# Kernel optimization log

Hardware: AMD Instinct MI355X
Metric: run time of the kernel (lower is better)

Reference implementation:

```python
import jax, jax.numpy as jnp
import numpy as np

B, S, D, H = 4, 2048, 1024, 16
HEAD_DIM = D // H
THETA = 10000.0
NEG_INF = -1e10


def apply_rope(x, theta=THETA):
    # RoPE over the FULL hid_dim (applied before head split, as in the torch code)
    d = x.shape[-1]
    s = x.shape[1]
    freqs = 1.0 / theta ** (jnp.arange(0, d, 2, dtype=jnp.float32) / d)  # [d/2]
    ang = jnp.arange(s, dtype=jnp.float32)[:, None] * freqs[None, :]     # [s, d/2]
    cos, sin = jnp.cos(ang), jnp.sin(ang)
    xr = x.reshape(x.shape[0], s, d // 2, 2)
    re, im = xr[..., 0], xr[..., 1]
    # complex multiply (re + i*im) * (cos + i*sin)
    out = jnp.stack([re * cos - im * sin, re * sin + im * cos], axis=-1)
    return out.reshape(x.shape)


def setup_inputs() -> dict:
    key = jax.random.key(0)
    ks = jax.random.split(key, 8)
    w_scale = 0.02
    return {
        "query": jax.random.normal(ks[0], (B, S, D), jnp.float32),
        "key": jax.random.normal(ks[1], (B, S, D), jnp.float32),
        "value": jax.random.normal(ks[2], (B, S, D), jnp.float32),
        "Wq": jax.random.normal(ks[3], (D, D), jnp.float32) * w_scale,
        "bq": jnp.zeros((D,), jnp.float32),
        "Wk": jax.random.normal(ks[4], (D, D), jnp.float32) * w_scale,
        "bk": jnp.zeros((D,), jnp.float32),
        "Wv": jax.random.normal(ks[5], (D, D), jnp.float32) * w_scale,
        "bv": jnp.zeros((D,), jnp.float32),
        "Wo": jax.random.normal(ks[6], (D, D), jnp.float32) * w_scale,
        "bo": jnp.zeros((D,), jnp.float32),
        "mask": jax.random.randint(ks[7], (B, 1, 1, S), 0, 2, jnp.int32),
    }


def reference(query, key, value, Wq, bq, Wk, bk, Wv, bv, Wo, bo, mask):
    b = query.shape[0]
    Q = query @ Wq + bq  # [B,Sq,D]
    K = key @ Wk + bk    # [B,Sk,D]
    V = value @ Wv + bv  # [B,Sk,D]
    Q = apply_rope(Q)
    K = apply_rope(K)
    # split heads: [B,H,S,head_dim]
    Qh = Q.reshape(b, -1, H, HEAD_DIM).transpose(0, 2, 1, 3)
    Kh = K.reshape(b, -1, H, HEAD_DIM).transpose(0, 2, 1, 3)
    Vh = V.reshape(b, -1, H, HEAD_DIM).transpose(0, 2, 1, 3)
    scale = 1.0 / jnp.sqrt(jnp.float32(HEAD_DIM))
    energy = jnp.einsum("bhqd,bhkd->bhqk", Qh, Kh) * scale
    energy = jnp.where(mask == 0, NEG_INF, energy)
    attn = jax.nn.softmax(energy, axis=-1)
    x = jnp.einsum("bhqk,bhkd->bhqd", attn, Vh)
    x = x.transpose(0, 2, 1, 3).reshape(b, -1, D)
    return x @ Wo + bo
```

## Files before the change

### kernel.cpp

```cpp
#include <hip/hip_runtime.h>
#include <math.h>

#define S_LEN 2048
#define DMODEL 1024
#define NHEAD 16
#define HDIM 64

typedef unsigned short ushort_t;
typedef __attribute__((ext_vector_type(8))) short short8;
typedef __attribute__((ext_vector_type(4))) float floatx4;
typedef __attribute__((ext_vector_type(4))) unsigned short ushort4v;
typedef __attribute__((ext_vector_type(2))) unsigned short ushort2v;

typedef __attribute__((address_space(3))) unsigned int lds_uint;
typedef const __attribute__((address_space(1))) unsigned int gbl_uint;

__device__ __forceinline__ float b2f(ushort_t u) {
  return __uint_as_float(((unsigned)u) << 16);
}
__device__ __forceinline__ ushort_t f2b(float x) {
  unsigned u = __float_as_uint(x);
  return (ushort_t)((u + 0x7fffu + ((u >> 16) & 1u)) >> 16);
}
__device__ __forceinline__ void gld16(const void* g, void* l) {
  __builtin_amdgcn_global_load_lds((gbl_uint*)g, (lds_uint*)l, 16, 0, 0);
}

__global__ __launch_bounds__(256) void detect_kernel(
    const unsigned* __restrict__ q, int* __restrict__ flag) {
  __shared__ int cnt[256];
  int c = 0;
#pragma unroll
  for (int i = 0; i < 16; ++i) {
    const unsigned w = q[threadIdx.x * 16 + i];
    const unsigned e = (w >> 7) & 0xFFu;
    c += (e >= 112u && e <= 135u) ? 1 : 0;
  }
  cnt[threadIdx.x] = c;
  __syncthreads();
  if (threadIdx.x == 0) {
    int t = 0;
    for (int i = 0; i < 256; ++i) t += cnt[i];
    *flag = (t > 2048) ? 1 : 0;
  }
}

__global__ __launch_bounds__(256) void bias_kernel(
    const void* __restrict__ bq, const void* __restrict__ bk,
    const void* __restrict__ bv, const void* __restrict__ bo,
    const int* __restrict__ flag, float* __restrict__ out) {
  const int i = blockIdx.x * 256 + threadIdx.x;
  const int z = i >> 10;
  const void* src = z == 0 ? bq : z == 1 ? bk : z == 2 ? bv : bo;
  const int j = i & 1023;
  const float v = (*flag) ? b2f(((const ushort_t*)src)[j])
                          : ((const float*)src)[j];
  out[i] = v;
}

__global__ __launch_bounds__(256) void wtrans_kernel(
    const void* __restrict__ Wq, const void* __restrict__ Wk,
    const void* __restrict__ Wv, const void* __restrict__ Wo,
    const int* __restrict__ flag, ushort_t* __restrict__ Wt) {
  __shared__ float t[32][33];
  const void* src = blockIdx.z == 0 ? Wq : blockIdx.z == 1 ? Wk
                    : blockIdx.z == 2 ? Wv : Wo;
  ushort_t* dst = Wt + (size_t)blockIdx.z * (DMODEL * (size_t)DMODEL);
  const int isbf = *flag;
  const int tx = threadIdx.x & 31, ty = threadIdx.x >> 5;
  const int bx = blockIdx.x * 32, by = blockIdx.y * 32;
#pragma unroll
  for (int i = 0; i < 4; ++i) {
    const size_t idx = (size_t)(by + ty + 8 * i) * DMODEL + bx + tx;
    t[ty + 8 * i][tx] = isbf ? b2f(((const ushort_t*)src)[idx])
                             : ((const float*)src)[idx];
  }
  __syncthreads();
#pragma unroll
  for (int i = 0; i < 4; ++i)
    dst[(size_t)(bx + ty + 8 * i) * DMODEL + by + tx] = f2b(t[tx][ty + 8 * i]);
}

__global__ __launch_bounds__(256) void qkv_kernel(
    const void* __restrict__ qin, const void* __restrict__ kin,
    const void* __restrict__ vin, const ushort_t* __restrict__ Wt,
    const float* __restrict__ Bias, const int* __restrict__ flag,
    ushort_t* __restrict__ Qh, ushort_t* __restrict__ Kh,
    ushort_t* __restrict__ Vh) {
  const int z = blockIdx.z;
  const void* A = z == 0 ? qin : z == 1 ? kin : vin;
  const ushort_t* W = Wt + (size_t)z * (DMODEL * (size_t)DMODEL);
  ushort_t* dst = z == 0 ? Qh : z == 1 ? Kh : Vh;
  const int isbf = *flag;

  __shared__ __align__(16) ushort_t smem[2 * 128 * 64];
  ushort_t* As = smem;
  ushort_t* Bs = smem + 128 * 64;

  const int tid = threadIdx.x;
  const int w = tid >> 6, l = tid & 63;
  const int m0 = blockIdx.x * 128, n0 = blockIdx.y * 128;

  floatx4 acc[4][4] = {};

  const int lr8 = l >> 3, lc8 = l & 7;
  const int gblk = lc8 ^ lr8;
  const ushort_t* Agb =
      (const ushort_t*)A + (size_t)(m0 + w * 32 + lr8) * DMODEL + gblk * 8;
  const float* Agf =
      (const float*)A + (size_t)(m0 + w * 32 + (l >> 4)) * DMODEL + (l & 15) * 4;
  const ushort_t* Bg = W + (size_t)(n0 + w * 32 + lr8) * DMODEL + gblk * 8;
  ushort_t* Asw = As + (w * 32) * 64;
  ushort_t* Bsw = Bs + (w * 32) * 64;

  const int wm = (w >> 1) * 64, wn = (w & 1) * 64;
  const int lm = l & 15, lg = l >> 4;
  const int swz = lm & 7;
  const int cA0 = ((0 + lg) ^ swz) * 8;
  const int cA1 = ((4 + lg) ^ swz) * 8;

  for (int kt = 0; kt < 16; ++kt) {
    const int ko = kt * 64;
    if (isbf) {
#pragma unroll
      for (int i = 0; i < 4; ++i)
        gld16(Agb + (size_t)(i * 8) * DMODEL + ko, Asw + (i * 8) * 64);
    } else {
#pragma unroll
      for (int i = 0; i < 8; ++i) {
        const floatx4 x = *(const floatx4*)(Agf + (size_t)(i * 4) * DMODEL + ko);
        ushort4v h;
        h[0] = f2b(x.x); h[1] = f2b(x.y); h[2] = f2b(x.z); h[3] = f2b(x.w);
        const int row = i * 4 + (l >> 4);
        const int blk = ((l & 15) >> 1) ^ (row & 7);
        *(ushort4v*)&Asw[row * 64 + blk * 8 + (l & 1) * 4] = h;
      }
    }
#pragma unroll
    for (int i = 0; i < 4; ++i)
      gld16(Bg + (size_t)(i * 8) * DMODEL + ko, Bsw + (i * 8) * 64);
    __syncthreads();
#pragma unroll
    for (int kk = 0; kk < 64; kk += 32) {
      const int ck = kk ? cA1 : cA0;
      short8 af[4], bf[4];
#pragma unroll
      for (int t = 0; t < 4; ++t)
        af[t] = *(const short8*)&As[(wm + t * 16 + lm) * 64 + ck];
#pragma unroll
      for (int t = 0; t < 4; ++t)
        bf[t] = *(const short8*)&Bs[(wn + t * 16 + lm) * 64 + ck];
#pragma unroll
      for (int mt = 0; mt < 4; ++mt)
#pragma unroll
        for (int nt = 0; nt < 4; ++nt)
          acc[mt][nt] = __builtin_amdgcn_mfma_f32_16x16x32_bf16(
              af[mt], bf[nt], acc[mt][nt], 0, 0, 0);
    }
    __syncthreads();
  }

  ushort_t* ep = smem + w * 4096;
#pragma unroll
  for (int nt = 0; nt < 4; ++nt) {
    const int c = nt * 16 + lm;
    const float bval = Bias[z * DMODEL + n0 + wn + c];
#pragma unroll
    for (int mt = 0; mt < 4; ++mt)
#pragma unroll
      for (int r = 0; r < 4; ++r) {
        const int row_t = mt * 16 + lg * 4 + r;
        ep[row_t * 64 + ((((c >> 3) ^ (row_t & 7)) << 3) | (c & 7))] =
            f2b(acc[mt][nt][r] + bval);
      }
  }
  const int mg = m0 + wm;
  const int b_ = mg >> 11, s_base = mg & (S_LEN - 1);
  const int h_ = (n0 + wn) >> 6;
  ushort_t* dstb = dst + (((size_t)(b_ * NHEAD + h_) * S_LEN + s_base) << 6);
#pragma unroll
  for (int i = 0; i < 8; ++i) {
    const int row = lr8 + 8 * i;
    const short8 v = *(const short8*)&ep[row * 64 + ((lc8 ^ lr8) << 3)];
    *(short8*)(dstb + (size_t)row * 64 + lc8 * 8) = v;
  }
}

__global__ __launch_bounds__(256) void rope_kernel(ushort_t* __restrict__ QK) {
  const size_t p = (size_t)blockIdx.x * 256 + threadIdx.x;
  const int d2 = (int)(p & 31) * 2;
  const int s = (int)(p >> 5) & (S_LEN - 1);
  const int h = (int)(p >> 16) & (NHEAD - 1);
  const int n = h * HDIM + d2;
  const float freq = exp2f((float)n * (-13.287712379549449f / 1024.0f));
  float sn, cs;
  __sincosf((float)s * freq, &sn, &cs);
  ushort2v v = *(ushort2v*)(QK + 2 * p);
  const float re = b2f(v[0]), im = b2f(v[1]);
  ushort2v o;
  o[0] = f2b(re * cs - im * sn);
  o[1] = f2b(re * sn + im * cs);
  *(ushort2v*)(QK + 2 * p) = o;
}

__global__ __launch_bounds__(256) void vtrans_kernel(
    const ushort_t* __restrict__ V, ushort_t* __restrict__ Vt) {
  __shared__ ushort_t t[32][34];
  const int bh = blockIdx.z;
  const int s0 = blockIdx.x * 32, d0 = blockIdx.y * 32;
  const ushort_t* src = V + (size_t)bh * S_LEN * HDIM;
  ushort_t* dst = Vt + (size_t)bh * S_LEN * HDIM;
  const int tx = threadIdx.x & 31, ty = threadIdx.x >> 5;
#pragma unroll
  for (int i = 0; i < 4; ++i)
    t[ty + 8 * i][tx] = src[(size_t)(s0 + ty + 8 * i) * HDIM + d0 + tx];
  __syncthreads();
#pragma unroll
  for (int i = 0; i < 4; ++i)
    dst[(size_t)(d0 + ty + 8 * i) * S_LEN + s0 + tx] = t[tx][ty + 8 * i];
}

__global__ __launch_bounds__(256) void attn_kernel(
    const ushort_t* __restrict__ Qh, const ushort_t* __restrict__ Kh,
    const ushort_t* __restrict__ Vt, const int* __restrict__ mask,
    ushort_t* __restrict__ Xa) {
  const int nlin = blockIdx.y * 16 + blockIdx.x;
  const int bh = ((nlin & 7) << 3) | ((nlin >> 3) & 7);
  const int q0 = (nlin >> 6) * 128;
  const int b = bh >> 4, h = bh & 15;
  const int tid = threadIdx.x;
  const int w = tid >> 6, lane = tid & 63;
  const int lm = lane & 15, lg = lane >> 4;

  __shared__ __align__(16) ushort_t Ks[64 * 64];
  __shared__ __align__(16) ushort_t Vs[64 * 64];
  __shared__ __align__(16) ushort_t Ps[4][32 * 72];

  const ushort_t* Qb = Qh + ((size_t)bh * S_LEN + q0 + w * 32) * HDIM;
  const ushort_t* Kb = Kh + (size_t)bh * S_LEN * HDIM;
  const ushort_t* Vb = Vt + (size_t)bh * S_LEN * HDIM;
  const int* mb = mask + b * S_LEN;

  short8 qf[2][2];
#pragma unroll
  for (int mb_ = 0; mb_ < 2; ++mb_)
#pragma unroll
    for (int ks = 0; ks < 2; ++ks)
      qf[mb_][ks] = *(const short8*)(Qb + (size_t)(mb_ * 16 + lm) * HDIM +
                                     ks * 32 + lg * 8);

  const int lr8 = lane >> 3, lc8 = lane & 7;
  const int gblk = lc8 ^ lr8;
  const ushort_t* Kg = Kb + (size_t)(w * 16 + lr8) * HDIM + gblk * 8;
  const ushort_t* Vg = Vb + (size_t)(w * 16 + lr8) * S_LEN + gblk * 8;
  ushort_t* KsW = Ks + (w * 16) * 64;
  ushort_t* VsW = Vs + (w * 16) * 64;

  const int swz = lm & 7;
  const int cK0 = ((0 + lg) ^ swz) * 8;
  const int cK1 = ((4 + lg) ^ swz) * 8;

  floatx4 Oacc[2][5] = {};

  const short8 ones = {0x3F80, 0x3F80, 0x3F80, 0x3F80,
                       0x3F80, 0x3F80, 0x3F80, 0x3F80};

  for (int j0 = 0; j0 < S_LEN; j0 += 64) {
    __syncthreads();
    gld16(Kg + (size_t)j0 * HDIM, KsW);
    gld16(Kg + (size_t)(j0 + 8) * HDIM, KsW + 8 * 64);
    gld16(Vg + j0, VsW);
    gld16(Vg + (size_t)8 * S_LEN + j0, VsW + 8 * 64);
    int mj[4];
#pragma unroll
    for (int nb = 0; nb < 4; ++nb) mj[nb] = mb[j0 + nb * 16 + lm];
    __syncthreads();

    floatx4 Sacc[2][4] = {};
#pragma unroll
    for (int ks = 0; ks < 2; ++ks) {
      const int ck = ks ? cK1 : cK0;
      short8 kf[4];
#pragma unroll
      for (int nb = 0; nb < 4; ++nb)
        kf[nb] = *(const short8*)&Ks[(nb * 16 + lm) * 64 + ck];
#pragma unroll
      for (int mb_ = 0; mb_ < 2; ++mb_)
#pragma unroll
        for (int nb = 0; nb < 4; ++nb)
          Sacc[mb_][nb] = __builtin_amdgcn_mfma_f32_16x16x32_bf16(
              qf[mb_][ks], kf[nb], Sacc[mb_][nb], 0, 0, 0);
    }

#pragma unroll
    for (int mb_ = 0; mb_ < 2; ++mb_)
#pragma unroll
      for (int nb = 0; nb < 4; ++nb)
#pragma unroll
        for (int r = 0; r < 4; ++r) {
          const float sv = Sacc[mb_][nb][r] * 0.125f;
          const float p = __expf(mj[nb] ? sv : -50.0f);
          Ps[w][(mb_ * 16 + lg * 4 + r) * 72 + nb * 16 + lm] = f2b(p);
        }

#pragma unroll
    for (int ks = 0; ks < 2; ++ks) {
      const int ck = ks ? cK1 : cK0;
      short8 pf[2], vf[4];
#pragma unroll
      for (int mb_ = 0; mb_ < 2; ++mb_)
        pf[mb_] =
            *(const short8*)&Ps[w][(mb_ * 16 + lm) * 72 + ks * 32 + lg * 8];
#pragma unroll
      for (int nb = 0; nb < 4; ++nb)
        vf[nb] = *(const short8*)&Vs[(nb * 16 + lm) * 64 + ck];
#pragma unroll
      for (int mb_ = 0; mb_ < 2; ++mb_) {
#pragma unroll
        for (int nb = 0; nb < 4; ++nb)
          Oacc[mb_][nb] = __builtin_amdgcn_mfma_f32_16x16x32_bf16(
              pf[mb_], vf[nb], Oacc[mb_][nb], 0, 0, 0);
        Oacc[mb_][4] = __builtin_amdgcn_mfma_f32_16x16x32_bf16(
            pf[mb_], ones, Oacc[mb_][4], 0, 0, 0);
      }
    }
  }

#pragma unroll
  for (int mb_ = 0; mb_ < 2; ++mb_)
#pragma unroll
    for (int r = 0; r < 4; ++r) {
      const float inv = 1.0f / Oacc[mb_][4][r];
      const int q = q0 + w * 32 + mb_ * 16 + lg * 4 + r;
      ushort_t* orow = Xa + (size_t)(b * S_LEN + q) * DMODEL + h * HDIM;
#pragma unroll
      for (int nb = 0; nb < 4; ++nb)
        orow[nb * 16 + lm] = f2b(Oacc[mb_][nb][r] * inv);
    }
}

__global__ __launch_bounds__(256) void oproj_kernel(
    const ushort_t* __restrict__ X, const ushort_t* __restrict__ Wt,
    const float* __restrict__ BiasO, const int* __restrict__ flag,
    void* __restrict__ out) {
  const int isbf = *flag;
  __shared__ __align__(16) ushort_t smem[2 * 128 * 64];
  ushort_t* As = smem;
  ushort_t* Bs = smem + 128 * 64;
  const int tid = threadIdx.x;
  const int w = tid >> 6, l = tid & 63;
  const int m0 = blockIdx.x * 128, n0 = blockIdx.y * 128;

  floatx4 acc[4][4] = {};

  const int lr8 = l >> 3, lc8 = l & 7;
  const int gblk = lc8 ^ lr8;
  const ushort_t* Ag =
      X + (size_t)(m0 + w * 32 + lr8) * DMODEL + gblk * 8;
  const ushort_t* Bg =
      Wt + (size_t)(n0 + w * 32 + lr8) * DMODEL + gblk * 8;
  ushort_t* Asw = As + (w * 32) * 64;
  ushort_t* Bsw = Bs + (w * 32) * 64;

  const int wm = (w >> 1) * 64, wn = (w & 1) * 64;
  const int lm = l & 15, lg = l >> 4;
  const int swz = lm & 7;
  const int cA0 = ((0 + lg) ^ swz) * 8;
  const int cA1 = ((4 + lg) ^ swz) * 8;

  for (int kt = 0; kt < 16; ++kt) {
    const int ko = kt * 64;
#pragma unroll
    for (int i = 0; i < 4; ++i) {
      gld16(Ag + (size_t)(i * 8) * DMODEL + ko, Asw + (i * 8) * 64);
      gld16(Bg + (size_t)(i * 8) * DMODEL + ko, Bsw + (i * 8) * 64);
    }
    __syncthreads();
#pragma unroll
    for (int kk = 0; kk < 64; kk += 32) {
      const int ck = kk ? cA1 : cA0;
      short8 af[4], bf[4];
#pragma unroll
      for (int t = 0; t < 4; ++t)
        af[t] = *(const short8*)&As[(wm + t * 16 + lm) * 64 + ck];
#pragma unroll
      for (int t = 0; t < 4; ++t)
        bf[t] = *(const short8*)&Bs[(wn + t * 16 + lm) * 64 + ck];
#pragma unroll
      for (int mt = 0; mt < 4; ++mt)
#pragma unroll
        for (int nt = 0; nt < 4; ++nt)
          acc[mt][nt] = __builtin_amdgcn_mfma_f32_16x16x32_bf16(
              af[mt], bf[nt], acc[mt][nt], 0, 0, 0);
    }
    __syncthreads();
  }

  if (isbf) {
    ushort_t* ep = smem + w * 4096;
#pragma unroll
    for (int nt = 0; nt < 4; ++nt) {
      const int c = nt * 16 + lm;
      const float bval = BiasO[n0 + wn + c];
#pragma unroll
      for (int mt = 0; mt < 4; ++mt)
#pragma unroll
        for (int r = 0; r < 4; ++r) {
          const int row_t = mt * 16 + lg * 4 + r;
          ep[row_t * 64 + ((((c >> 3) ^ (row_t & 7)) << 3) | (c & 7))] =
              f2b(acc[mt][nt][r] + bval);
        }
    }
    ushort_t* outb = (ushort_t*)out + (size_t)(m0 + wm) * DMODEL + n0 + wn;
#pragma unroll
    for (int i = 0; i < 8; ++i) {
      const int row = lr8 + 8 * i;
      const short8 v = *(const short8*)&ep[row * 64 + ((lc8 ^ lr8) << 3)];
      *(short8*)(outb + (size_t)row * DMODEL + lc8 * 8) = v;
    }
  } else {
    const int lr = lg * 4;
#pragma unroll
    for (int nt = 0; nt < 4; ++nt) {
      const int n_g = n0 + wn + nt * 16 + lm;
      const float bval = BiasO[n_g];
#pragma unroll
      for (int mt = 0; mt < 4; ++mt)
#pragma unroll
        for (int r = 0; r < 4; ++r) {
          const int m_g = m0 + wm + mt * 16 + lr + r;
          ((float*)out)[(size_t)m_g * DMODEL + n_g] = acc[mt][nt][r] + bval;
        }
    }
  }
}

extern "C" void kernel_launch(void* const* d_in, const int* in_sizes, int n_in,
                              void* d_out, int out_size, void* d_ws,
                              size_t ws_size, hipStream_t stream) {
  char* ws = (char*)d_ws;
  const size_t MB = 1024 * 1024;
  int* flag = (int*)ws;
  float* Bias = (float*)(ws + 4096);
  ushort_t* Wt = (ushort_t*)(ws + 1 * MB);
  ushort_t* Qh = (ushort_t*)(ws + 16 * MB);
  ushort_t* Kh = (ushort_t*)(ws + 32 * MB);
  ushort_t* Vh = (ushort_t*)(ws + 48 * MB);
  ushort_t* Vt = (ushort_t*)(ws + 64 * MB);
  ushort_t* Xa = Vh;

  detect_kernel<<<1, 256, 0, stream>>>((const unsigned*)d_in[0], flag);
  bias_kernel<<<16, 256, 0, stream>>>(d_in[4], d_in[6], d_in[8], d_in[10],
                                      flag, Bias);
  wtrans_kernel<<<dim3(32, 32, 4), 256, 0, stream>>>(d_in[3], d_in[5], d_in[7],
                                                     d_in[9], flag, Wt);
  qkv_kernel<<<dim3(64, 8, 3), 256, 0, stream>>>(d_in[0], d_in[1], d_in[2], Wt,
                                                 Bias, flag, Qh, Kh, Vh);
  rope_kernel<<<32768, 256, 0, stream>>>(Qh);
  vtrans_kernel<<<dim3(64, 2, 64), 256, 0, stream>>>(Vh, Vt);
  attn_kernel<<<dim3(16, 64), 256, 0, stream>>>(Qh, Kh, Vt,
                                                (const int*)d_in[11], Xa);
  oproj_kernel<<<dim3(64, 8), 256, 0, stream>>>(
      Xa, Wt + (size_t)3 * DMODEL * DMODEL, Bias + 3 * DMODEL, flag, d_out);
}
```

Before: 440.6 us.

## Add pre-converted bf16 inputs and 256x256 pipelined QKV GEMM kernel

Adds a convert pass that writes q/k/v as bf16 into workspace, then replaces the 128-tile QKV projection with a 256x256-tile, 512-thread GEMM. The new GEMM double-buffers global-to-LDS loads with explicit waitcnt/barrier scheduling, uses a swizzled LDS layout and block-index swizzling, and writes head-split output through an LDS-staged epilogue. The aim is more data reuse per tile and better MFMA utilisation. In exchange it spends an extra pass and bandwidth on conversion, and the path runs only when the workspace is at least 128MB.

```diff
diff --git a/kernel.cpp b/kernel.cpp
--- a/kernel.cpp
+++ b/kernel.cpp
@@ -79,6 +79,207 @@
 #pragma unroll
   for (int i = 0; i < 4; ++i)
     dst[(size_t)(bx + ty + 8 * i) * DMODEL + by + tx] = f2b(t[tx][ty + 8 * i]);
+}
+
+__global__ __launch_bounds__(256) void convert_kernel(
+    const void* __restrict__ q, const void* __restrict__ k,
+    const void* __restrict__ v, const int* __restrict__ flag,
+    ushort_t* __restrict__ Abf) {
+  const int z = blockIdx.y;
+  const void* src = z == 0 ? q : z == 1 ? k : v;
+  ushort_t* dst = Abf + (size_t)z * (8192 * (size_t)DMODEL);
+  const size_t i = (size_t)blockIdx.x * 256 + threadIdx.x;
+  short8 o;
+  if (*flag) {
+    o = ((const short8*)src)[i];
+  } else {
+    const floatx4 a = ((const floatx4*)src)[2 * i];
+    const floatx4 b = ((const floatx4*)src)[2 * i + 1];
+    o[0] = (short)f2b(a.x); o[1] = (short)f2b(a.y);
+    o[2] = (short)f2b(a.z); o[3] = (short)f2b(a.w);
+    o[4] = (short)f2b(b.x); o[5] = (short)f2b(b.y);
+    o[6] = (short)f2b(b.z); o[7] = (short)f2b(b.w);
+  }
+  ((short8*)dst)[i] = o;
+}
+
+__device__ __forceinline__ void gemm256_core(
+    const ushort_t* __restrict__ A, const ushort_t* __restrict__ Bm,
+    const int m0, const int n0, ushort_t* smem, floatx4 acc[8][4]) {
+  const int tid = threadIdx.x;
+  const int w = tid >> 6, l = tid & 63;
+  const int wr = w >> 2, wc = w & 3;
+  const int lm = l & 15, lg = l >> 4;
+  const int lr8 = l >> 3, lc8 = l & 7;
+  const int gblk = lc8 ^ lr8;
+
+  ushort_t* Ab = smem;
+  ushort_t* Bb = smem + 32768;
+
+  const ushort_t* Ag = A + (size_t)(m0 + w * 16 + lr8) * DMODEL + gblk * 8;
+  const ushort_t* Bg = Bm + (size_t)(n0 + w * 16 + lr8) * DMODEL + gblk * 8;
+  ushort_t* Asw = Ab + (w * 16) * 64;
+  ushort_t* Bsw = Bb + (w * 16) * 64;
+
+  const int swz = lm & 7;
+  const int cK0 = ((0 + lg) ^ swz) * 8;
+  const int cK1 = ((4 + lg) ^ swz) * 8;
+
+  short8 af[4][2], bf0[2][2], bf1[2][2];
+
+#define FENCE asm volatile("" ::: "memory")
+#define BAR                        \
+  do {                             \
+    FENCE;                         \
+    __builtin_amdgcn_s_barrier();  \
+    FENCE;                         \
+  } while (0)
+#define STG(gp, lp, h, ko)                                                    \
+  do {                                                                        \
+    gld16((gp) + (size_t)((h) * 128) * DMODEL + (ko),                         \
+          (lp) + ((h) * 128) * 64);                                           \
+    gld16((gp) + (size_t)((h) * 128 + 8) * DMODEL + (ko),                     \
+          (lp) + ((h) * 128 + 8) * 64);                                       \
+  } while (0)
+#define LDA(mh, co)                                                           \
+  do {                                                                        \
+    _Pragma("unroll") for (int f = 0; f < 4; ++f) {                           \
+      const int ra = (co) + (wr * 128 + (mh) * 64 + f * 16 + lm) * 64;        \
+      af[f][0] = *(const short8*)&Ab[ra + cK0];                               \
+      af[f][1] = *(const short8*)&Ab[ra + cK1];                               \
+    }                                                                         \
+  } while (0)
+#define LDB(bfx, nh, co)                                                      \
+  do {                                                                        \
+    _Pragma("unroll") for (int f = 0; f < 2; ++f) {                           \
+      const int rb = (co) + (wc * 64 + (nh) * 32 + f * 16 + lm) * 64;         \
+      bfx[f][0] = *(const short8*)&Bb[rb + cK0];                              \
+      bfx[f][1] = *(const short8*)&Bb[rb + cK1];                              \
+    }                                                                         \
+  } while (0)
+#define MMA(mh, nh, bfx)                                                      \
+  do {                                                                        \
+    __builtin_amdgcn_s_setprio(1);                                            \
+    _Pragma("unroll") for (int ks = 0; ks < 2; ++ks)                          \
+    _Pragma("unroll") for (int f = 0; f < 4; ++f)                             \
+    _Pragma("unroll") for (int f2 = 0; f2 < 2; ++f2)                          \
+      acc[(mh) * 4 + f][(nh) * 2 + f2] =                                      \
+          __builtin_amdgcn_mfma_f32_16x16x32_bf16(                            \
+              af[f][ks], bfx[f2][ks], acc[(mh) * 4 + f][(nh) * 2 + f2],       \
+              0, 0, 0);                                                       \
+    __builtin_amdgcn_s_setprio(0);                                            \
+  } while (0)
+
+  STG(Ag, Asw, 0, 0);
+  STG(Bg, Bsw, 0, 0);
+  STG(Bg, Bsw, 1, 0);
+  STG(Ag, Asw, 1, 0);
+  asm volatile("s_waitcnt vmcnt(4)" ::: "memory");
+  BAR;
+
+  for (int t = 0; t < 15; ++t) {
+    const int co = (t & 1) << 14;
+    const int so = ((t + 1) & 1) << 14;
+    const int ko = (t + 1) * 64;
+    LDA(0, co);
+    LDB(bf0, 0, co);
+    STG(Ag, Asw + so, 0, ko);
+    STG(Bg, Bsw + so, 0, ko);
+    BAR;
+    MMA(0, 0, bf0);
+    asm volatile("s_waitcnt vmcnt(6)" ::: "memory");
+    BAR;
+    LDB(bf1, 1, co);
+    STG(Bg, Bsw + so, 1, ko);
+    BAR;
+    MMA(0, 1, bf1);
+    asm volatile("s_waitcnt vmcnt(6)" ::: "memory");
+    BAR;
+    LDA(1, co);
+    STG(Ag, Asw + so, 1, ko);
+    BAR;
+    MMA(1, 0, bf0);
+    BAR;
+    MMA(1, 1, bf1);
+    asm volatile("s_waitcnt vmcnt(4)" ::: "memory");
+    BAR;
+  }
+  {
+    const int co = 1 << 14;
+    LDA(0, co);
+    LDB(bf0, 0, co);
+    BAR;
+    MMA(0, 0, bf0);
+    asm volatile("s_waitcnt vmcnt(2)" ::: "memory");
+    BAR;
+    LDB(bf1, 1, co);
+    BAR;
+    MMA(0, 1, bf1);
+    asm volatile("s_waitcnt vmcnt(0)" ::: "memory");
+    BAR;
+    LDA(1, co);
+    BAR;
+    MMA(1, 0, bf0);
+    BAR;
+    MMA(1, 1, bf1);
+    BAR;
+  }
+#undef MMA
+#undef LDB
+#undef LDA
+#undef STG
+#undef BAR
+#undef FENCE
+}
+
+__global__ __launch_bounds__(512, 2) void qkv256_kernel(
+    const ushort_t* __restrict__ Abf, const ushort_t* __restrict__ Wt,
+    const float* __restrict__ Bias, ushort_t* __restrict__ Qh,
+    ushort_t* __restrict__ Kh, ushort_t* __restrict__ Vh) {
+  __shared__ __align__(16) ushort_t smem[65536];
+  const int bid = blockIdx.x;
+  const int sw = (bid & 7) * 48 + (bid >> 3);
+  const int z = sw >> 7;
+  const int tt = sw & 127;
+  const int m0 = (tt >> 2) * 256, n0 = (tt & 3) * 256;
+  const ushort_t* A = Abf + (size_t)z * (8192 * (size_t)DMODEL);
+  const ushort_t* B = Wt + (size_t)z * (DMODEL * (size_t)DMODEL);
+
+  floatx4 acc[8][4] = {};
+  gemm256_core(A, B, m0, n0, smem, acc);
+
+  const int tid = threadIdx.x;
+  const int w = tid >> 6, l = tid & 63;
+  const int wr = w >> 2, wc = w & 3;
+  const int lm = l & 15, lg = l >> 4;
+  const int lr8 = l >> 3, lc8 = l & 7;
+  ushort_t* dst = z == 0 ? Qh : z == 1 ? Kh : Vh;
+
+  ushort_t* ep = smem + w * 8192;
+  const int n_base = n0 + wc * 64;
+#pragma unroll
+  for (int nf = 0; nf < 4; ++nf) {
+    const int c = nf * 16 + lm;
+    const float bval = Bias[z * DMODEL + n_base + c];
+#pragma unroll
+    for (int mf = 0; mf < 8; ++mf)
+#pragma unroll
+      for (int r = 0; r < 4; ++r) {
+        const int rowt = mf * 16 + lg * 4 + r;
+        ep[rowt * 64 + ((((c >> 3) ^ (rowt & 7)) << 3) | (c & 7))] =
+            f2b(acc[mf][nf][r] + bval);
+      }
+  }
+  const int mg = m0 + wr * 128;
+  const int b_ = mg >> 11, s_base = mg & (S_LEN - 1);
+  const int h_ = n_base >> 6;
+  ushort_t* dstb = dst + (((size_t)(b_ * NHEAD + h_) * S_LEN + s_base) << 6);
+#pragma unroll
+  for (int i = 0; i < 16; ++i) {
+    const int row = lr8 + 8 * i;
+    const short8 v2 = *(const short8*)&ep[row * 64 + ((lc8 ^ lr8) << 3)];
+    *(short8*)(dstb + ((size_t)row << 6) + lc8 * 8) = v2;
+  }
 }
 
 __global__ __launch_bounds__(256) void qkv_kernel(
@@ -447,15 +648,24 @@
   ushort_t* Kh = (ushort_t*)(ws + 32 * MB);
   ushort_t* Vh = (ushort_t*)(ws + 48 * MB);
   ushort_t* Vt = (ushort_t*)(ws + 64 * MB);
+  ushort_t* Abf = (ushort_t*)(ws + 80 * MB);
   ushort_t* Xa = Vh;
+
+  const int use256 = ws_size >= (size_t)128 * MB;
 
   detect_kernel<<<1, 256, 0, stream>>>((const unsigned*)d_in[0], flag);
   bias_kernel<<<16, 256, 0, stream>>>(d_in[4], d_in[6], d_in[8], d_in[10],
                                       flag, Bias);
   wtrans_kernel<<<dim3(32, 32, 4), 256, 0, stream>>>(d_in[3], d_in[5], d_in[7],
                                                      d_in[9], flag, Wt);
-  qkv_kernel<<<dim3(64, 8, 3), 256, 0, stream>>>(d_in[0], d_in[1], d_in[2], Wt,
-                                                 Bias, flag, Qh, Kh, Vh);
+  if (use256) {
+    convert_kernel<<<dim3(4096, 3), 256, 0, stream>>>(d_in[0], d_in[1],
+                                                      d_in[2], flag, Abf);
+    qkv256_kernel<<<384, 512, 0, stream>>>(Abf, Wt, Bias, Qh, Kh, Vh);
+  } else {
+    qkv_kernel<<<dim3(64, 8, 3), 256, 0, stream>>>(d_in[0], d_in[1], d_in[2],
+                                                   Wt, Bias, flag, Qh, Kh, Vh);
+  }
   rope_kernel<<<32768, 256, 0, stream>>>(Qh);
   vtrans_kernel<<<dim3(64, 2, 64), 256, 0, stream>>>(Vh, Vt);
   attn_kernel<<<dim3(16, 64), 256, 0, stream>>>(Qh, Kh, Vt,
```

Result: faster. 402.7 us (-8.6%).
